# Kernel tuning notes

Measured on AMD Instinct MI355X. Metric: run time of the kernel, lower is better.

## Reference

```python
import jax, jax.numpy as jnp
import numpy as np

N_NODES = 50000
N_EDGES = 800000
NUM_GRAPHS = 250
NODES_PER_GRAPH = 200  # max_len for to_dense_batch
IN_DIM = 128
H1 = 128
H2 = 128
LSTM_H = 128
OUT_DIM = 2
NEG_SLOPE = 0.2  # PyG GATConv default leaky relu slope


def setup_inputs() -> dict:
    key = jax.random.key(0)
    ks = jax.random.split(key, 16)
    x = jax.random.normal(ks[0], (N_NODES, IN_DIM), dtype=jnp.float32)
    edge_index = jax.random.randint(ks[1], (2, N_EDGES), 0, N_NODES, dtype=jnp.int32)
    batch = (jnp.arange(N_NODES, dtype=jnp.int32) // NODES_PER_GRAPH)
    g = lambda k, shp, fan: jax.random.normal(k, shp, dtype=jnp.float32) / np.sqrt(fan)
    return {
        "x": x,
        "edge_index": edge_index,
        "batch": batch,
        "W_gat": g(ks[2], (IN_DIM, H1), IN_DIM),
        "a_src": g(ks[3], (H1,), H1),
        "a_dst": g(ks[4], (H1,), H1),
        "b_gat": jnp.zeros((H1,), jnp.float32),
        "W_gcn": g(ks[5], (H1, H2), H1),
        "b_gcn": jnp.zeros((H2,), jnp.float32),
        "W_ih": g(ks[6], (4 * LSTM_H, H2), H2),
        "W_hh": g(ks[7], (4 * LSTM_H, LSTM_H), LSTM_H),
        "b_ih": jnp.zeros((4 * LSTM_H,), jnp.float32),
        "b_hh": jnp.zeros((4 * LSTM_H,), jnp.float32),
        "W_fc": g(ks[8], (LSTM_H, OUT_DIM), LSTM_H),
        "b_fc": jnp.zeros((OUT_DIM,), jnp.float32),
    }


def _add_self_loops(edge_index, n):
    loop = jnp.arange(n, dtype=edge_index.dtype)
    src = jnp.concatenate([edge_index[0], loop])
    dst = jnp.concatenate([edge_index[1], loop])
    return src, dst


def _gat_conv(x, edge_index, W, a_src, a_dst, b):
    n = x.shape[0]
    h = x @ W                                  # [N, H1]
    src, dst = _add_self_loops(edge_index, n)
    alpha_s = h @ a_src                        # [N]
    alpha_d = h @ a_dst
    e = alpha_s[src] + alpha_d[dst]            # [E+N]
    e = jnp.where(e > 0, e, NEG_SLOPE * e)     # leaky relu
    # softmax over edges sharing the same destination node
    m = jax.ops.segment_max(e, dst, num_segments=n)
    ex = jnp.exp(e - m[dst])
    denom = jax.ops.segment_sum(ex, dst, num_segments=n)
    alpha = ex / denom[dst]
    out = jax.ops.segment_sum(h[src] * alpha[:, None], dst, num_segments=n)
    return out + b


def _gcn_conv(x, edge_index, W, b):
    n = x.shape[0]
    h = x @ W                                  # [N, H2]
    src, dst = _add_self_loops(edge_index, n)
    deg = jax.ops.segment_sum(jnp.ones_like(dst, dtype=h.dtype), dst, num_segments=n)
    dinv = jax.lax.rsqrt(jnp.maximum(deg, 1.0))
    coef = dinv[src] * dinv[dst]               # symmetric normalization
    out = jax.ops.segment_sum(h[src] * coef[:, None], dst, num_segments=n)
    return out + b


def _to_dense_batch(x, batch, num_graphs, max_len):
    n = x.shape[0]
    ones = jnp.ones((n,), jnp.int32)
    counts = jax.ops.segment_sum(ones, batch, num_segments=num_graphs)
    starts = jnp.cumsum(counts) - counts
    pos = jnp.arange(n, dtype=jnp.int32) - starts[batch]
    padded = jnp.zeros((num_graphs, max_len, x.shape[1]), x.dtype)
    padded = padded.at[batch, pos].set(x)
    return padded, counts


def _lstm_last_hidden(padded, lengths, W_ih, W_hh, b_ih, b_hh):
    B, T, D = padded.shape
    H = W_hh.shape[1]
    xs = jnp.swapaxes(padded, 0, 1)            # [T, B, D]

    def step(carry, x_t):
        h, c = carry
        gates = x_t @ W_ih.T + b_ih + h @ W_hh.T + b_hh
        i, f, g, o = jnp.split(gates, 4, axis=-1)
        c = jax.nn.sigmoid(f) * c + jax.nn.sigmoid(i) * jnp.tanh(g)
        h = jax.nn.sigmoid(o) * jnp.tanh(c)
        return (h, c), h

    init = (jnp.zeros((B, H), padded.dtype), jnp.zeros((B, H), padded.dtype))
    _, hs = jax.lax.scan(step, init, xs)       # hs: [T, B, H]
    # packed-sequence semantics: hidden state at each graph's last valid step
    return hs[lengths - 1, jnp.arange(B)]


def reference(x, edge_index, batch, W_gat, a_src, a_dst, b_gat, W_gcn, b_gcn,
              W_ih, W_hh, b_ih, b_hh, W_fc, b_fc):
    h = jax.nn.relu(_gat_conv(x, edge_index, W_gat, a_src, a_dst, b_gat))
    h = jax.nn.relu(_gcn_conv(h, edge_index, W_gcn, b_gcn))
    padded, lengths = _to_dense_batch(h, batch, NUM_GRAPHS, NODES_PER_GRAPH)
    g_rep = _lstm_last_hidden(padded, lengths, W_ih, W_hh, b_ih, b_hh)
    return g_rep @ W_fc + b_fc
```

## Files before the change

### kernel.cpp

```cpp
#include <hip/hip_runtime.h>
#include <cstddef>

#define NN 50000
#define NE 800000
#define NG 250
#define TT 200
#define DD 128
#define GH 512
#define NEG_SLOPE 0.2f
#define NCHUNK 4
#define CLEN 50
#define CAP 128
#define PSTRIDE 136

typedef __attribute__((ext_vector_type(8))) short bf16x8;
typedef __attribute__((ext_vector_type(4))) float f32x4;

static __device__ __forceinline__ float fsig(float x) { return 1.0f / (1.0f + __expf(-x)); }
static __device__ __forceinline__ float ftanh(float x) {
    float e = __expf(2.0f * x);
    return 1.0f - 2.0f / (e + 1.0f);
}
static __device__ __forceinline__ unsigned short f2bf(float f) {
    unsigned int u = __float_as_uint(f);
    return (unsigned short)((u + 0x7fffu + ((u >> 16) & 1u)) >> 16);
}
static __device__ __forceinline__ float bf2f(unsigned short b) {
    return __uint_as_float(((unsigned int)b) << 16);
}

static __device__ __forceinline__ void gll16(const float* src, float* ldsdst) {
    __builtin_amdgcn_global_load_lds(
        (const __attribute__((address_space(1))) void*)src,
        (__attribute__((address_space(3))) void*)ldsdst, 16, 0, 0);
}

__global__ void k_init(int* cnt, int* gstart, int n, int ng1) {
    int i = blockIdx.x * 256 + threadIdx.x;
    if (i < n) cnt[i] = 1;
    if (i < ng1) gstart[i] = n;
}

__global__ void k_transpose2(const float* __restrict__ inA, float* __restrict__ outA,
                             const float* __restrict__ inB, float* __restrict__ outB) {
    int b = blockIdx.x, k = threadIdx.x;
    if (b < DD) outA[b * DD + k] = inA[k * DD + b];
    else { int n = b - DD; outB[n * DD + k] = inB[k * DD + n]; }
}

__global__ __launch_bounds__(256) void k_gemm(
    const float* __restrict__ A, const float* __restrict__ B, float* __restrict__ C,
    int M, int N, int t0, int clen, int rowsPerGraph,
    const float* __restrict__ bias1, const float* __restrict__ bias2,
    unsigned short* __restrict__ Cbf,
    float* __restrict__ as_out, float* __restrict__ ad_out,
    const float* __restrict__ a_src, const float* __restrict__ a_dst)
{
    __shared__ float4 As[2][1024];
    __shared__ float4 Bs[2][1024];
    const int tid = threadIdx.x;
    const int wv = tid >> 6;
    const int m0 = blockIdx.x * 128, n0 = blockIdx.y * 128;
    const int tr = tid >> 4, tc = tid & 15;

    float acc[8][8];
    #pragma unroll
    for (int i = 0; i < 8; ++i)
        #pragma unroll
        for (int j = 0; j < 8; ++j) acc[i][j] = 0.f;

    auto stageA = [&](int buf, int k0) {
        #pragma unroll
        for (int it = 0; it < 4; ++it) {
            int f4 = it * 256 + tid;
            int r = f4 >> 3;
            int c4s = (f4 & 7) ^ (r & 7);
            int gr = m0 + r;
            float* dst = (float*)&As[buf][it * 256 + wv * 64];
            if (gr < M) {
                int flat = (gr / clen) * rowsPerGraph + t0 + (gr % clen);
                gll16(A + (size_t)flat * DD + k0 + c4s * 4, dst);
            }
        }
    };
    auto stageB = [&](int buf, int k0) {
        #pragma unroll
        for (int it = 0; it < 4; ++it) {
            int f4 = it * 256 + tid;
            int r = f4 >> 3;
            int c4s = (f4 & 7) ^ (r & 7);
            int gn = n0 + r;
            float* dst = (float*)&Bs[buf][it * 256 + wv * 64];
            if (gn < N) gll16(B + (size_t)gn * DD + k0 + c4s * 4, dst);
        }
    };

    stageA(0, 0); stageB(0, 0);
    __syncthreads();
    int buf = 0;
    const int axor = tr & 7;
    const int bxor = tc & 7;
    for (int ks = 0; ks < 4; ++ks) {
        if (ks < 3) { stageA(buf ^ 1, (ks + 1) * 32); stageB(buf ^ 1, (ks + 1) * 32); }
        const float4* Af = &As[buf][0];
        const float4* Bf = &Bs[buf][0];
        #pragma unroll 1
        for (int k4 = 0; k4 < 8; ++k4) {
            float4 a[8], b[8];
            #pragma unroll
            for (int i = 0; i < 8; ++i) a[i] = Af[(tr + i * 16) * 8 + (k4 ^ axor)];
            #pragma unroll
            for (int j = 0; j < 8; ++j) b[j] = Bf[(tc + j * 16) * 8 + (k4 ^ bxor)];
            #pragma unroll
            for (int i = 0; i < 8; ++i)
                #pragma unroll
                for (int j = 0; j < 8; ++j)
                    acc[i][j] += a[i].x * b[j].x + a[i].y * b[j].y + a[i].z * b[j].z + a[i].w * b[j].w;
        }
        __syncthreads();
        buf ^= 1;
    }

    if (as_out) {
        float asv[8], adv[8];
        #pragma unroll
        for (int j = 0; j < 8; ++j) { asv[j] = a_src[tc + 16 * j]; adv[j] = a_dst[tc + 16 * j]; }
        #pragma unroll
        for (int i = 0; i < 8; ++i) {
            float s = 0.f, d = 0.f;
            #pragma unroll
            for (int j = 0; j < 8; ++j) { s += acc[i][j] * asv[j]; d += acc[i][j] * adv[j]; }
            #pragma unroll
            for (int off = 1; off < 16; off <<= 1) { s += __shfl_xor(s, off); d += __shfl_xor(d, off); }
            int gr = m0 + tr + i * 16;
            if (tc == 0 && gr < M) { as_out[gr] = s; ad_out[gr] = d; }
        }
    }

    #pragma unroll
    for (int i = 0; i < 8; ++i) {
        int gr = m0 + tr + i * 16;
        if (gr >= M) continue;
        #pragma unroll
        for (int j = 0; j < 8; ++j) {
            int gn = n0 + tc + j * 16;
            if (gn >= N) continue;
            float v = acc[i][j];
            if (bias1) v += bias1[gn];
            if (bias2) v += bias2[gn];
            if (Cbf) Cbf[(size_t)gr * N + gn] = f2bf(v);
            else     C[(size_t)gr * N + gn] = v;
        }
    }
}

__global__ __launch_bounds__(256) void k_gemm_mx(
    const float* __restrict__ A, const float* __restrict__ Bw, float* __restrict__ C,
    int M, int N, const float* __restrict__ bias1, const float* __restrict__ bias2)
{
    __shared__ float4 As[4096];
    const int tid = threadIdx.x;
    const int wv = tid >> 6;
    const int l = tid & 63;
    const int m0 = blockIdx.x * 128, n0 = blockIdx.y * 128;
    const int wr = (wv >> 1) * 64, wc = (wv & 1) * 64;
    const int lr = l & 15, kg = l >> 4;

    #pragma unroll
    for (int it = 0; it < 16; ++it) {
        int f4 = it * 256 + tid;
        int r = f4 >> 5, c4 = f4 & 31;
        int c4s = c4 ^ (r & 7);
        int gr = m0 + r;
        float* dst = (float*)&As[it * 256 + wv * 64];
        if (gr < M) gll16(A + (size_t)gr * DD + c4s * 4, dst);
    }

    bf16x8 bh[4][4];
    #pragma unroll
    for (int ct = 0; ct < 4; ++ct) {
        const float* brow = Bw + (size_t)(n0 + wc + ct * 16 + lr) * DD;
        #pragma unroll
        for (int ks = 0; ks < 4; ++ks) {
            float4 f0 = *(const float4*)(brow + ks * 32 + kg * 8);
            float4 f1 = *(const float4*)(brow + ks * 32 + kg * 8 + 4);
            float ff[8] = {f0.x, f0.y, f0.z, f0.w, f1.x, f1.y, f1.z, f1.w};
            #pragma unroll
            for (int j = 0; j < 8; ++j) bh[ct][ks][j] = (short)f2bf(ff[j]);
        }
    }
    __syncthreads();

    f32x4 acc[4][4];
    #pragma unroll
    for (int rt = 0; rt < 4; ++rt)
        #pragma unroll
        for (int ct = 0; ct < 4; ++ct) acc[rt][ct] = (f32x4){0.f, 0.f, 0.f, 0.f};

    #pragma unroll 1
    for (int ks = 0; ks < 4; ++ks) {
        bf16x8 ahi[4], alo[4];
        #pragma unroll
        for (int rt = 0; rt < 4; ++rt) {
            int row = wr + rt * 16 + lr;
            int qb = ks * 8 + kg * 2;
            float4 f0 = As[row * 32 + (qb ^ (row & 7))];
            float4 f1 = As[row * 32 + ((qb + 1) ^ (row & 7))];
            float ff[8] = {f0.x, f0.y, f0.z, f0.w, f1.x, f1.y, f1.z, f1.w};
            #pragma unroll
            for (int j = 0; j < 8; ++j) {
                unsigned short hi = f2bf(ff[j]);
                ahi[rt][j] = (short)hi;
                alo[rt][j] = (short)f2bf(ff[j] - bf2f(hi));
            }
        }
        #pragma unroll
        for (int rt = 0; rt < 4; ++rt)
            #pragma unroll
            for (int ct = 0; ct < 4; ++ct) {
                acc[rt][ct] = __builtin_amdgcn_mfma_f32_16x16x32_bf16(ahi[rt], bh[ct][ks], acc[rt][ct], 0, 0, 0);
                acc[rt][ct] = __builtin_amdgcn_mfma_f32_16x16x32_bf16(alo[rt], bh[ct][ks], acc[rt][ct], 0, 0, 0);
            }
    }

    #pragma unroll
    for (int ct = 0; ct < 4; ++ct) {
        const float* brow = Bw + (size_t)(n0 + wc + ct * 16 + lr) * DD;
        #pragma unroll
        for (int ks = 0; ks < 4; ++ks) {
            float4 f0 = *(const float4*)(brow + ks * 32 + kg * 8);
            float4 f1 = *(const float4*)(brow + ks * 32 + kg * 8 + 4);
            float ff[8] = {f0.x, f0.y, f0.z, f0.w, f1.x, f1.y, f1.z, f1.w};
            #pragma unroll
            for (int j = 0; j < 8; ++j)
                bh[ct][ks][j] = (short)f2bf(ff[j] - bf2f(f2bf(ff[j])));
        }
    }

    #pragma unroll 1
    for (int ks = 0; ks < 4; ++ks) {
        bf16x8 ahi[4];
        #pragma unroll
        for (int rt = 0; rt < 4; ++rt) {
            int row = wr + rt * 16 + lr;
            int qb = ks * 8 + kg * 2;
            float4 f0 = As[row * 32 + (qb ^ (row & 7))];
            float4 f1 = As[row * 32 + ((qb + 1) ^ (row & 7))];
            float ff[8] = {f0.x, f0.y, f0.z, f0.w, f1.x, f1.y, f1.z, f1.w};
            #pragma unroll
            for (int j = 0; j < 8; ++j) ahi[rt][j] = (short)f2bf(ff[j]);
        }
        #pragma unroll
        for (int rt = 0; rt < 4; ++rt)
            #pragma unroll
            for (int ct = 0; ct < 4; ++ct)
                acc[rt][ct] = __builtin_amdgcn_mfma_f32_16x16x32_bf16(ahi[rt], bh[ct][ks], acc[rt][ct], 0, 0, 0);
    }

    #pragma unroll
    for (int ct = 0; ct < 4; ++ct) {
        int col = n0 + wc + ct * 16 + lr;
        float bsum = bias1[col] + bias2[col];
        #pragma unroll
        for (int rt = 0; rt < 4; ++rt) {
            #pragma unroll
            for (int r = 0; r < 4; ++r) {
                int row = m0 + wr + rt * 16 + kg * 4 + r;
                if (row < M) C[(size_t)row * N + col] = acc[rt][ct][r] + bsum;
            }
        }
    }
}

__global__ __launch_bounds__(256) void k_gemm_mx128(
    const float* __restrict__ A, const float* __restrict__ Bw,
    unsigned short* __restrict__ Cbf, int M,
    float* __restrict__ as_out, float* __restrict__ ad_out,
    const float* __restrict__ a_src, const float* __restrict__ a_dst)
{
    __shared__ float4 As[4096];
    const int tid = threadIdx.x;
    const int wv = tid >> 6;
    const int l = tid & 63;
    const int lr = l & 15, kg = l >> 4;
    const int m0 = blockIdx.x * 128;
    const int rowbase = wv * 32;

    #pragma unroll
    for (int it = 0; it < 16; ++it) {
        int f4 = it * 256 + tid;
        int r = f4 >> 5, c4 = f4 & 31;
        int c4s = c4 ^ (r & 7);
        int gr = m0 + r;
        float* dst = (float*)&As[it * 256 + wv * 64];
        if (gr < M) gll16(A + (size_t)gr * DD + c4s * 4, dst);
    }
    __syncthreads();

    f32x4 acc[2][8];
    #pragma unroll
    for (int rt = 0; rt < 2; ++rt)
        #pragma unroll
        for (int ct = 0; ct < 8; ++ct) acc[rt][ct] = (f32x4){0.f, 0.f, 0.f, 0.f};

    #pragma unroll 1
    for (int ks = 0; ks < 4; ++ks) {
        bf16x8 bh[8];
        #pragma unroll
        for (int ct = 0; ct < 8; ++ct) {
            const float* brow = Bw + (size_t)(ct * 16 + lr) * DD + ks * 32 + kg * 8;
            float4 f0 = *(const float4*)brow;
            float4 f1 = *(const float4*)(brow + 4);
            float ff[8] = {f0.x, f0.y, f0.z, f0.w, f1.x, f1.y, f1.z, f1.w};
            #pragma unroll
            for (int j = 0; j < 8; ++j) bh[ct][j] = (short)f2bf(ff[j]);
        }
        bf16x8 ahi[2], alo[2];
        #pragma unroll
        for (int rt = 0; rt < 2; ++rt) {
            int row = rowbase + rt * 16 + lr;
            int qb = ks * 8 + kg * 2;
            float4 f0 = As[row * 32 + (qb ^ (row & 7))];
            float4 f1 = As[row * 32 + ((qb + 1) ^ (row & 7))];
            float ff[8] = {f0.x, f0.y, f0.z, f0.w, f1.x, f1.y, f1.z, f1.w};
            #pragma unroll
            for (int j = 0; j < 8; ++j) {
                unsigned short hi = f2bf(ff[j]);
                ahi[rt][j] = (short)hi;
                alo[rt][j] = (short)f2bf(ff[j] - bf2f(hi));
            }
        }
        #pragma unroll
        for (int rt = 0; rt < 2; ++rt)
            #pragma unroll
            for (int ct = 0; ct < 8; ++ct) {
                acc[rt][ct] = __builtin_amdgcn_mfma_f32_16x16x32_bf16(ahi[rt], bh[ct], acc[rt][ct], 0, 0, 0);
                acc[rt][ct] = __builtin_amdgcn_mfma_f32_16x16x32_bf16(alo[rt], bh[ct], acc[rt][ct], 0, 0, 0);
            }
    }
    #pragma unroll 1
    for (int ks = 0; ks < 4; ++ks) {
        bf16x8 bl[8];
        #pragma unroll
        for (int ct = 0; ct < 8; ++ct) {
            const float* brow = Bw + (size_t)(ct * 16 + lr) * DD + ks * 32 + kg * 8;
            float4 f0 = *(const float4*)brow;
            float4 f1 = *(const float4*)(brow + 4);
            float ff[8] = {f0.x, f0.y, f0.z, f0.w, f1.x, f1.y, f1.z, f1.w};
            #pragma unroll
            for (int j = 0; j < 8; ++j)
                bl[ct][j] = (short)f2bf(ff[j] - bf2f(f2bf(ff[j])));
        }
        bf16x8 ahi[2];
        #pragma unroll
        for (int rt = 0; rt < 2; ++rt) {
            int row = rowbase + rt * 16 + lr;
            int qb = ks * 8 + kg * 2;
            float4 f0 = As[row * 32 + (qb ^ (row & 7))];
            float4 f1 = As[row * 32 + ((qb + 1) ^ (row & 7))];
            float ff[8] = {f0.x, f0.y, f0.z, f0.w, f1.x, f1.y, f1.z, f1.w};
            #pragma unroll
            for (int j = 0; j < 8; ++j) ahi[rt][j] = (short)f2bf(ff[j]);
        }
        #pragma unroll
        for (int rt = 0; rt < 2; ++rt)
            #pragma unroll
            for (int ct = 0; ct < 8; ++ct)
                acc[rt][ct] = __builtin_amdgcn_mfma_f32_16x16x32_bf16(ahi[rt], bl[ct], acc[rt][ct], 0, 0, 0);
    }

    #pragma unroll
    for (int rt = 0; rt < 2; ++rt)
        #pragma unroll
        for (int ct = 0; ct < 8; ++ct) {
            int row = m0 + rowbase + rt * 16 + kg * 4;
            int col = ct * 16 + lr;
            #pragma unroll
            for (int r = 0; r < 4; ++r)
                if (row + r < M) Cbf[(size_t)(row + r) * DD + col] = f2bf(acc[rt][ct][r]);
        }
    if (as_out) {
        #pragma unroll
        for (int rt = 0; rt < 2; ++rt)
            #pragma unroll
            for (int r = 0; r < 4; ++r) {
                float s = 0.f, d = 0.f;
                #pragma unroll
                for (int ct = 0; ct < 8; ++ct) {
                    int col = ct * 16 + lr;
                    s += acc[rt][ct][r] * a_src[col];
                    d += acc[rt][ct][r] * a_dst[col];
                }
                #pragma unroll
                for (int off = 1; off < 16; off <<= 1) {
                    s += __shfl_xor(s, off);
                    d += __shfl_xor(d, off);
                }
                int row = m0 + rowbase + rt * 16 + kg * 4 + r;
                if (lr == 0 && row < M) { as_out[row] = s; ad_out[row] = d; }
            }
    }
}

__global__ void k_hist(const int* __restrict__ ei, int* cnt, int E) {
    int e = blockIdx.x * 256 + threadIdx.x;
    if (e < E) atomicAdd(&cnt[ei[E + e]], 1);
}

__global__ __launch_bounds__(256) void k_scan1(const int* __restrict__ cnt, int* __restrict__ fill,
                                               int* __restrict__ bsum, int n) {
    __shared__ int wsum[4];
    int tid = threadIdx.x, lane = tid & 63, wv = tid >> 6;
    int i = blockIdx.x * 256 + tid;
    int v = (i < n) ? cnt[i] : 0;
    int sc = v;
    #pragma unroll
    for (int off = 1; off < 64; off <<= 1) {
        int t = __shfl_up(sc, off);
        if (lane >= off) sc += t;
    }
    if (lane == 63) wsum[wv] = sc;
    __syncthreads();
    int base = 0;
    if (wv > 0) base += wsum[0];
    if (wv > 1) base += wsum[1];
    if (wv > 2) base += wsum[2];
    if (i < n) fill[i] = base + sc - v;
    if (tid == 255) bsum[blockIdx.x] = base + sc;
}
__global__ __launch_bounds__(256) void k_scan2(int* __restrict__ bsum, int nb) {
    __shared__ int wsum[4];
    int tid = threadIdx.x, lane = tid & 63, wv = tid >> 6;
    int v = (tid < nb) ? bsum[tid] : 0;
    int sc = v;
    #pragma unroll
    for (int off = 1; off < 64; off <<= 1) {
        int t = __shfl_up(sc, off);
        if (lane >= off) sc += t;
    }
    if (lane == 63) wsum[wv] = sc;
    __syncthreads();
    int base = 0;
    if (wv > 0) base += wsum[0];
    if (wv > 1) base += wsum[1];
    if (wv > 2) base += wsum[2];
    if (tid < nb) bsum[tid] = base + sc - v;
}
__global__ void k_scan3(const int* __restrict__ bsum, const int* __restrict__ cnt,
                        int* __restrict__ rp, int* __restrict__ fill,
                        float* __restrict__ dinv, const int* __restrict__ batch,
                        int* __restrict__ gstart, int n) {
    int i = blockIdx.x * 256 + threadIdx.x;
    if (i >= n) return;
    int v = fill[i] + bsum[blockIdx.x];
    rp[i] = v;
    fill[i] = v;
    if (i == n - 1) rp[n] = v + cnt[i];
    dinv[i] = rsqrtf(fmaxf((float)cnt[i], 1.0f));
    int b = batch[i];
    if (i == 0 || batch[i - 1] != b) gstart[b] = i;
}

__global__ void k_fill(const int* __restrict__ ei, int* fill, int* esrc, int E, int N) {
    int i = blockIdx.x * 256 + threadIdx.x;
    if (i < E) {
        int s = ei[i], d = ei[E + i];
        int slot = atomicAdd(&fill[d], 1);
        esrc[slot] = s;
    } else if (i < E + N) {
        int v = i - E;
        int slot = atomicAdd(&fill[v], 1);
        esrc[slot] = v;
    }
}

__global__ __launch_bounds__(256) void k_gat(
    const unsigned int* __restrict__ h1b,
    const float* __restrict__ as, const float* __restrict__ ad_,
    const int* __restrict__ rp, const int* __restrict__ esrc,
    const float* __restrict__ bias, float* __restrict__ out, int n)
{
    __shared__ float2 ws_sh[4][CAP];
    int wv = threadIdx.x >> 6;
    int node = blockIdx.x * 4 + wv;
    int lane = threadIdx.x & 63;
    if (node >= n) return;
    int r0 = rp[node], r1 = rp[node + 1];
    int deg = r1 - r0;
    float adv = ad_[node];

    float sum = 0.f;
    for (int base = 0; base < deg; base += 64) {
        int idx = base + lane;
        float ex = 0.f;
        if (idx < deg) {
            int s = esrc[r0 + idx];
            float e = as[s] + adv;
            e = e > 0.f ? e : NEG_SLOPE * e;
            ex = __expf(e);
            if (idx < CAP) ws_sh[wv][idx] = make_float2(ex, __int_as_float(s));
        }
        sum += ex;
    }
    #pragma unroll
    for (int off = 1; off < 64; off <<= 1) sum += __shfl_xor(sum, off);
    float inv = 1.0f / sum;

    int nser = deg < CAP ? deg : CAP;
    int npad = (nser + 7) & ~7;
    for (int p = nser + lane; p < npad; p += 64)
        ws_sh[wv][p] = make_float2(0.f, __int_as_float(0));

    float ax = 0.f, ay = 0.f;
    float wa[8]; unsigned int va[8];
    #pragma unroll
    for (int u = 0; u < 8; ++u) {
        float2 t = ws_sh[wv][u];
        wa[u] = t.x; va[u] = h1b[(size_t)__float_as_int(t.y) * 64 + lane];
    }
    #pragma unroll 1
    for (int idx = 8; idx < npad; idx += 8) {
        float wb[8]; unsigned int vb[8];
        #pragma unroll
        for (int u = 0; u < 8; ++u) {
            float2 t = ws_sh[wv][idx + u];
            wb[u] = t.x; vb[u] = h1b[(size_t)__float_as_int(t.y) * 64 + lane];
        }
        #pragma unroll
        for (int u = 0; u < 8; ++u) {
            ax += wa[u] * __uint_as_float(va[u] << 16);
            ay += wa[u] * __uint_as_float(va[u] & 0xffff0000u);
        }
        #pragma unroll
        for (int u = 0; u < 8; ++u) { wa[u] = wb[u]; va[u] = vb[u]; }
    }
    #pragma unroll
    for (int u = 0; u < 8; ++u) {
        ax += wa[u] * __uint_as_float(va[u] << 16);
        ay += wa[u] * __uint_as_float(va[u] & 0xffff0000u);
    }

    for (int j = r0 + CAP; j < r1; ++j) {
        int s = esrc[j];
        float e = as[s] + adv;
        e = e > 0.f ? e : NEG_SLOPE * e;
        float w = __expf(e);
        unsigned int v = h1b[(size_t)s * 64 + lane];
        ax += w * __uint_as_float(v << 16);
        ay += w * __uint_as_float(v & 0xffff0000u);
    }
    float2 bv = *(const float2*)(bias + 2 * lane);
    float2 o;
    o.x = fmaxf(ax * inv + bv.x, 0.f);
    o.y = fmaxf(ay * inv + bv.y, 0.f);
    *(float2*)(out + (size_t)node * DD + 2 * lane) = o;
}

__global__ __launch_bounds__(256) void k_gcn(
    const unsigned int* __restrict__ h2b, const float* __restrict__ dinv,
    const int* __restrict__ rp, const int* __restrict__ esrc,
    const float* __restrict__ bias, const int* __restrict__ batch,
    const int* __restrict__ gstart, float* __restrict__ padded, int n)
{
    __shared__ float2 cs_sh[4][CAP];
    int wv = threadIdx.x >> 6;
    int node = blockIdx.x * 4 + wv;
    int lane = threadIdx.x & 63;
    if (node >= n) return;
    int r0 = rp[node], r1 = rp[node + 1];
    int deg = r1 - r0;
    float dn = dinv[node];

    for (int base = 0; base < deg; base += 64) {
        int idx = base + lane;
        if (idx < deg && idx < CAP) {
            int s = esrc[r0 + idx];
            cs_sh[wv][idx] = make_float2(dinv[s], __int_as_float(s));
        }
    }
    int nser = deg < CAP ? deg : CAP;
    int npad = (nser + 7) & ~7;
    for (int p = nser + lane; p < npad; p += 64)
        cs_sh[wv][p] = make_float2(0.f, __int_as_float(0));
    __syncthreads();

    float ax = 0.f, ay = 0.f;
    float wa[8]; unsigned int va[8];
    #pragma unroll
    for (int u = 0; u < 8; ++u) {
        float2 t = cs_sh[wv][u];
        wa[u] = t.x; va[u] = h2b[(size_t)__float_as_int(t.y) * 64 + lane];
    }
    #pragma unroll 1
    for (int idx = 8; idx < npad; idx += 8) {
        float wb[8]; unsigned int vb[8];
        #pragma unroll
        for (int u = 0; u < 8; ++u) {
            float2 t = cs_sh[wv][idx + u];
            wb[u] = t.x; vb[u] = h2b[(size_t)__float_as_int(t.y) * 64 + lane];
        }
        #pragma unroll
        for (int u = 0; u < 8; ++u) {
            ax += wa[u] * __uint_as_float(va[u] << 16);
            ay += wa[u] * __uint_as_float(va[u] & 0xffff0000u);
        }
        #pragma unroll
        for (int u = 0; u < 8; ++u) { wa[u] = wb[u]; va[u] = vb[u]; }
    }
    #pragma unroll
    for (int u = 0; u < 8; ++u) {
        ax += wa[u] * __uint_as_float(va[u] << 16);
        ay += wa[u] * __uint_as_float(va[u] & 0xffff0000u);
    }

    for (int j = r0 + CAP; j < r1; ++j) {
        int s = esrc[j];
        float c = dinv[s];
        unsigned int v = h2b[(size_t)s * 64 + lane];
        ax += c * __uint_as_float(v << 16);
        ay += c * __uint_as_float(v & 0xffff0000u);
    }
    int g = batch[node];
    if (g < 0 || g >= NG) return;
    int p = node - gstart[g];
    if (p < 0 || p >= TT) return;
    float2 bv = *(const float2*)(bias + 2 * lane);
    float2 o;
    o.x = fmaxf(ax * dn + bv.x, 0.f);
    o.y = fmaxf(ay * dn + bv.y, 0.f);
    *(float2*)(padded + ((size_t)g * TT + p) * DD + 2 * lane) = o;
}

__global__ __launch_bounds__(1024) void k_lstm8(
    const float* __restrict__ xw,
    const float* __restrict__ Whh,
    const int* __restrict__ gstart,
    float* __restrict__ grep)
{
    int g = blockIdx.x, tid = threadIdx.x;
    __shared__ __align__(16) float h_sh[DD];
    __shared__ __align__(16) float part[8][4 * PSTRIDE];

    const int seg = tid >> 7;
    const int gq  = tid & 127;
    const int qt  = gq >> 5;
    const int ub  = (gq & 31) * 4;
    const int u   = tid >> 2;
    const int q   = tid & 3;
    const int lane = tid & 63;
    const int qbase = lane & ~3;

    float4 w[4][4];
    #pragma unroll
    for (int g4 = 0; g4 < 4; ++g4)
        #pragma unroll
        for (int i = 0; i < 4; ++i)
            w[g4][i] = *(const float4*)(Whh + (size_t)(4 * gq + g4) * DD + seg * 16 + i * 4);

    float creg = 0.f, hn = 0.f;
    if (tid < DD) h_sh[tid] = 0.f;
    int take = gstart[g + 1] - gstart[g] - 1;
    if (take < 0) take = 0;
    if (take > TT - 1) take = TT - 1;
    __syncthreads();

    const float* xb = xw + (size_t)g * TT * GH + q * DD + (u & 127);
    float xv = (tid < 512) ? xb[0] : 0.f;

    for (int t = 0; t < TT; ++t) {
        float xvn = 0.f;
        if (tid < 512 && t + 1 < TT) xvn = xb[(size_t)(t + 1) * GH];

        float4 hseg[4];
        #pragma unroll
        for (int i = 0; i < 4; ++i) hseg[i] = *(const float4*)(h_sh + seg * 16 + i * 4);
        float p0 = 0.f, p1 = 0.f, p2 = 0.f, p3 = 0.f;
        #pragma unroll
        for (int i = 0; i < 4; ++i) {
            float4 h4 = hseg[i];
            p0 += h4.x * w[0][i].x + h4.y * w[0][i].y + h4.z * w[0][i].z + h4.w * w[0][i].w;
            p1 += h4.x * w[1][i].x + h4.y * w[1][i].y + h4.z * w[1][i].z + h4.w * w[1][i].w;
            p2 += h4.x * w[2][i].x + h4.y * w[2][i].y + h4.z * w[2][i].z + h4.w * w[2][i].w;
            p3 += h4.x * w[3][i].x + h4.y * w[3][i].y + h4.z * w[3][i].z + h4.w * w[3][i].w;
        }
        *(float4*)(&part[seg][qt * PSTRIDE + ub]) = make_float4(p0, p1, p2, p3);
        __syncthreads();

        if (tid < 512) {
            int pidx = q * PSTRIDE + u;
            float G = xv + ((part[0][pidx] + part[1][pidx]) + (part[2][pidx] + part[3][pidx]))
                         + ((part[4][pidx] + part[5][pidx]) + (part[6][pidx] + part[7][pidx]));
            float a = (q == 2) ? 2.f : -1.f;
            float e = __expf(a * G);
            float act = (q == 2) ? (1.f - 2.f / (e + 1.f)) : (1.f / (1.f + e));
            float ai = __shfl(act, qbase + 0);
            float af = __shfl(act, qbase + 1);
            float ag = __shfl(act, qbase + 2);
            float ao = __shfl(act, qbase + 3);
            creg = af * creg + ai * ag;
            hn = ao * ftanh(creg);
            if (q == 0) {
                h_sh[u] = hn;
                if (t == take) grep[g * DD + u] = hn;
            }
        }
        xv = xvn;
        __syncthreads();
    }
}

__global__ __launch_bounds__(512) void k_lstm(
    const float* __restrict__ xw, const float* __restrict__ Whh,
    const int* __restrict__ gstart,
    float* __restrict__ hstate, float* __restrict__ cstate,
    float* __restrict__ grep, int t0, int clen)
{
    int g = blockIdx.x, tid = threadIdx.x;
    __shared__ __align__(16) float h_sh[DD];
    __shared__ __align__(16) float part[4][4 * PSTRIDE];

    const int seg = tid >> 7;
    const int gq  = tid & 127;
    const int qt  = gq >> 5;
    const int ub  = (gq & 31) * 4;
    const int u   = tid >> 2;
    const int q   = tid & 3;
    const int lane = tid & 63;
    const int qbase = lane & ~3;

    float4 w[4][8];
    #pragma unroll
    for (int g4 = 0; g4 < 4; ++g4)
        #pragma unroll
        for (int i = 0; i < 8; ++i)
            w[g4][i] = *(const float4*)(Whh + (size_t)(4 * gq + g4) * DD + seg * 32 + i * 4);

    float creg = 0.f, hn = 0.f;
    if (t0 == 0) {
        if (tid < DD) h_sh[tid] = 0.f;
    } else {
        creg = cstate[g * DD + u];
        hn = hstate[g * DD + u];
        if (q == 0) h_sh[u] = hn;
    }
    int take = gstart[g + 1] - gstart[g] - 1;
    if (take < 0) take = 0;
    if (take > TT - 1) take = TT - 1;
    __syncthreads();

    const float* xb = xw + (size_t)g * clen * GH + q * DD + u;
    float xv = xb[0];

    for (int t = t0; t < t0 + clen; ++t) {
        int rel = t - t0;
        float xvn = 0.f;
        if (rel + 1 < clen) xvn = xb[(size_t)(rel + 1) * GH];

        float4 hseg[8];
        #pragma unroll
        for (int i = 0; i < 8; ++i) hseg[i] = *(const float4*)(h_sh + seg * 32 + i * 4);
        float p0 = 0.f, p1 = 0.f, p2 = 0.f, p3 = 0.f;
        #pragma unroll
        for (int i = 0; i < 8; ++i) {
            float4 h4 = hseg[i];
            p0 += h4.x * w[0][i].x + h4.y * w[0][i].y + h4.z * w[0][i].z + h4.w * w[0][i].w;
            p1 += h4.x * w[1][i].x + h4.y * w[1][i].y + h4.z * w[1][i].z + h4.w * w[1][i].w;
            p2 += h4.x * w[2][i].x + h4.y * w[2][i].y + h4.z * w[2][i].z + h4.w * w[2][i].w;
            p3 += h4.x * w[3][i].x + h4.y * w[3][i].y + h4.z * w[3][i].z + h4.w * w[3][i].w;
        }
        *(float4*)(&part[seg][qt * PSTRIDE + ub]) = make_float4(p0, p1, p2, p3);
        __syncthreads();

        int pidx = q * PSTRIDE + u;
        float G = xv + part[0][pidx] + part[1][pidx] + part[2][pidx] + part[3][pidx];
        float a = (q == 2) ? 2.f : -1.f;
        float e = __expf(a * G);
        float act = (q == 2) ? (1.f - 2.f / (e + 1.f)) : (1.f / (1.f + e));
        float ai = __shfl(act, qbase + 0);
        float af = __shfl(act, qbase + 1);
        float ag = __shfl(act, qbase + 2);
        float ao = __shfl(act, qbase + 3);
        creg = af * creg + ai * ag;
        hn = ao * ftanh(creg);
        if (q == 0) {
            h_sh[u] = hn;
            if (t == take) grep[g * DD + u] = hn;
        }
        xv = xvn;
        __syncthreads();
    }
    if (q == 0) { hstate[g * DD + u] = hn; cstate[g * DD + u] = creg; }
}

__global__ void k_fc(const float* __restrict__ grep, const float* __restrict__ Wfc,
                     const float* __restrict__ bfc, float* __restrict__ out, int G) {
    int i = blockIdx.x * 256 + threadIdx.x;
    if (i >= G * 2) return;
    int g = i >> 1, o = i & 1;
    float acc = bfc[o];
    for (int d = 0; d < DD; ++d) acc += grep[g * DD + d] * Wfc[d * 2 + o];
    out[i] = acc;
}

extern "C" void kernel_launch(void* const* d_in, const int* in_sizes, int n_in,
                              void* d_out, int out_size, void* d_ws, size_t ws_size,
                              hipStream_t stream) {
    const float* x     = (const float*)d_in[0];
    const int*   ei    = (const int*)d_in[1];
    const int*   batch = (const int*)d_in[2];
    const float* Wgat  = (const float*)d_in[3];
    const float* a_src = (const float*)d_in[4];
    const float* a_dst = (const float*)d_in[5];
    const float* b_gat = (const float*)d_in[6];
    const float* Wgcn  = (const float*)d_in[7];
    const float* b_gcn = (const float*)d_in[8];
    const float* Wih   = (const float*)d_in[9];
    const float* Whh   = (const float*)d_in[10];
    const float* b_ih  = (const float*)d_in[11];
    const float* b_hh  = (const float*)d_in[12];
    const float* Wfc   = (const float*)d_in[13];
    const float* b_fc  = (const float*)d_in[14];
    float* out = (float*)d_out;

    float* ws = (float*)d_ws;
    const size_t F = (size_t)NN * DD;
    unsigned short* h1b = (unsigned short*)ws;
    unsigned short* h2b = (unsigned short*)ws;
    float* xwChunk = ws;
    float* gato   = ws + F;
    float* padded = ws + F;
    size_t off = 2 * F;
    float* alpha_s = ws + off; off += 50048;
    float* alpha_d = ws + off; off += 50048;
    float* dinv    = ws + off; off += 50048;
    int*   cnt     = (int*)(ws + off); off += 50048;
    int*   rp      = (int*)(ws + off); off += 50056;
    int*   fill    = (int*)(ws + off); off += 50048;
    int*   esrc    = (int*)(ws + off); off += 850048;
    int*   bsum    = (int*)(ws + off); off += 256;
    int*   gstart  = (int*)(ws + off); off += 256;
    float* grep    = ws + off; off += 32000;
    float* hstate  = ws + off; off += 32000;
    float* cstate  = ws + off; off += 32000;
    float* WgatT   = ws + off; off += 16384;
    float* WgcnT   = ws + off; off += 16384;
    const size_t xwBigFloats = (size_t)NG * TT * GH;
    float* xwBig = ws + off;
    const bool big = ws_size >= (off + xwBigFloats) * sizeof(float);

    k_transpose2<<<256, 128, 0, stream>>>(Wgat, WgatT, Wgcn, WgcnT);

    if (big) {
        k_gemm_mx128<<<391, 256, 0, stream>>>(x, WgatT, h1b, NN,
                                              alpha_s, alpha_d, a_src, a_dst);
    } else {
        k_gemm<<<dim3(391, 1), 256, 0, stream>>>(x, WgatT, nullptr, NN, DD, 0, TT, TT,
                                                 nullptr, nullptr, h1b,
                                                 alpha_s, alpha_d, a_src, a_dst);
    }

    k_init<<<196, 256, 0, stream>>>(cnt, gstart, NN, NG + 1);
    k_hist<<<3125, 256, 0, stream>>>(ei, cnt, NE);
    k_scan1<<<196, 256, 0, stream>>>(cnt, fill, bsum, NN);
    k_scan2<<<1, 256, 0, stream>>>(bsum, 196);
    k_scan3<<<196, 256, 0, stream>>>(bsum, cnt, rp, fill, dinv, batch, gstart, NN);
    k_fill<<<3321, 256, 0, stream>>>(ei, fill, esrc, NE, NN);

    k_gat<<<12500, 256, 0, stream>>>((const unsigned int*)h1b, alpha_s, alpha_d,
                                     rp, esrc, b_gat, gato, NN);

    if (big) {
        k_gemm_mx128<<<391, 256, 0, stream>>>(gato, WgcnT, h2b, NN,
                                              nullptr, nullptr, nullptr, nullptr);
    } else {
        k_gemm<<<dim3(391, 1), 256, 0, stream>>>(gato, WgcnT, nullptr, NN, DD, 0, TT, TT,
                                                 nullptr, nullptr, h2b,
                                                 nullptr, nullptr, nullptr, nullptr);
    }

    k_gcn<<<12500, 256, 0, stream>>>((const unsigned int*)h2b, dinv, rp, esrc,
                                     b_gcn, batch, gstart, padded, NN);

    if (big) {
        k_gemm_mx<<<dim3(391, 4), 256, 0, stream>>>(padded, Wih, xwBig, NG * TT, GH,
                                                    b_ih, b_hh);
        k_lstm8<<<NG, 1024, 0, stream>>>(xwBig, Whh, gstart, grep);
    } else {
        for (int c = 0; c < NCHUNK; ++c) {
            int t0 = c * CLEN;
            k_gemm<<<dim3(98, 4), 256, 0, stream>>>(padded, Wih, xwChunk, NG * CLEN, GH,
                                                    t0, CLEN, TT, b_ih, b_hh,
                                                    nullptr, nullptr, nullptr, nullptr, nullptr);
            k_lstm<<<NG, 512, 0, stream>>>(xwChunk, Whh, gstart, hstate, cstate, grep, t0, CLEN);
        }
    }

    k_fc<<<2, 256, 0, stream>>>(grep, Wfc, b_fc, out, NG);
}
```

Before: 559.6 us.

## Loop GEMM over all output column groups per block and stage stores via LDS

The input-projection GEMM now launches one block per 128-row tile and loops over all four 128-column groups, so the A tile is loaded into LDS once instead of four times across separate blocks. Results are staged through a padded LDS buffer so global stores are coalesced float4 row writes. The 1024-thread LSTM kernel is removed and the big path uses the 512-thread LSTM kernel over the full sequence. This cuts grid parallelism to 391 blocks and raises LDS use per block, which may lower occupancy.

```diff
diff --git a/kernel.cpp b/kernel.cpp
--- a/kernel.cpp
+++ b/kernel.cpp
@@ -12,6 +12,7 @@
 #define CLEN 50
 #define CAP 128
 #define PSTRIDE 136
+#define CSTRIDE 132
 
 typedef __attribute__((ext_vector_type(8))) short bf16x8;
 typedef __attribute__((ext_vector_type(4))) float f32x4;
@@ -156,13 +157,14 @@
 
 __global__ __launch_bounds__(256) void k_gemm_mx(
     const float* __restrict__ A, const float* __restrict__ Bw, float* __restrict__ C,
-    int M, int N, const float* __restrict__ bias1, const float* __restrict__ bias2)
+    int M, const float* __restrict__ bias1, const float* __restrict__ bias2)
 {
     __shared__ float4 As[4096];
+    __shared__ float  Cs[128 * CSTRIDE];
     const int tid = threadIdx.x;
     const int wv = tid >> 6;
     const int l = tid & 63;
-    const int m0 = blockIdx.x * 128, n0 = blockIdx.y * 128;
+    const int m0 = blockIdx.x * 128;
     const int wr = (wv >> 1) * 64, wc = (wv & 1) * 64;
     const int lr = l & 15, kg = l >> 4;
 
@@ -175,99 +177,109 @@
         float* dst = (float*)&As[it * 256 + wv * 64];
         if (gr < M) gll16(A + (size_t)gr * DD + c4s * 4, dst);
     }
-
-    bf16x8 bh[4][4];
-    #pragma unroll
-    for (int ct = 0; ct < 4; ++ct) {
-        const float* brow = Bw + (size_t)(n0 + wc + ct * 16 + lr) * DD;
-        #pragma unroll
+    __syncthreads();
+
+    #pragma unroll 1
+    for (int cg = 0; cg < 4; ++cg) {
+        const int n0 = cg * 128;
+        f32x4 acc[4][4];
+        #pragma unroll
+        for (int rt = 0; rt < 4; ++rt)
+            #pragma unroll
+            for (int ct = 0; ct < 4; ++ct) acc[rt][ct] = (f32x4){0.f, 0.f, 0.f, 0.f};
+
+        bf16x8 bh[4][4];
+        #pragma unroll
+        for (int ct = 0; ct < 4; ++ct) {
+            const float* brow = Bw + (size_t)(n0 + wc + ct * 16 + lr) * DD;
+            #pragma unroll
+            for (int ks = 0; ks < 4; ++ks) {
+                float4 f0 = *(const float4*)(brow + ks * 32 + kg * 8);
+                float4 f1 = *(const float4*)(brow + ks * 32 + kg * 8 + 4);
+                float ff[8] = {f0.x, f0.y, f0.z, f0.w, f1.x, f1.y, f1.z, f1.w};
+                #pragma unroll
+                for (int j = 0; j < 8; ++j) bh[ct][ks][j] = (short)f2bf(ff[j]);
+            }
+        }
+        #pragma unroll 1
         for (int ks = 0; ks < 4; ++ks) {
-            float4 f0 = *(const float4*)(brow + ks * 32 + kg * 8);
-            float4 f1 = *(const float4*)(brow + ks * 32 + kg * 8 + 4);
-            float ff[8] = {f0.x, f0.y, f0.z, f0.w, f1.x, f1.y, f1.z, f1.w};
-            #pragma unroll
-            for (int j = 0; j < 8; ++j) bh[ct][ks][j] = (short)f2bf(ff[j]);
-        }
-    }
-    __syncthreads();
-
-    f32x4 acc[4][4];
-    #pragma unroll
-    for (int rt = 0; rt < 4; ++rt)
-        #pragma unroll
-        for (int ct = 0; ct < 4; ++ct) acc[rt][ct] = (f32x4){0.f, 0.f, 0.f, 0.f};
-
-    #pragma unroll 1
-    for (int ks = 0; ks < 4; ++ks) {
-        bf16x8 ahi[4], alo[4];
-        #pragma unroll
-        for (int rt = 0; rt < 4; ++rt) {
-            int row = wr + rt * 16 + lr;
-            int qb = ks * 8 + kg * 2;
-            float4 f0 = As[row * 32 + (qb ^ (row & 7))];
-            float4 f1 = As[row * 32 + ((qb + 1) ^ (row & 7))];
-            float ff[8] = {f0.x, f0.y, f0.z, f0.w, f1.x, f1.y, f1.z, f1.w};
-            #pragma unroll
-            for (int j = 0; j < 8; ++j) {
-                unsigned short hi = f2bf(ff[j]);
-                ahi[rt][j] = (short)hi;
-                alo[rt][j] = (short)f2bf(ff[j] - bf2f(hi));
+            bf16x8 ahi[4], alo[4];
+            #pragma unroll
+            for (int rt = 0; rt < 4; ++rt) {
+                int row = wr + rt * 16 + lr;
+                int qb = ks * 8 + kg * 2;
+                float4 f0 = As[row * 32 + (qb ^ (row & 7))];
+                float4 f1 = As[row * 32 + ((qb + 1) ^ (row & 7))];
+                float ff[8] = {f0.x, f0.y, f0.z, f0.w, f1.x, f1.y, f1.z, f1.w};
+                #pragma unroll
+                for (int j = 0; j < 8; ++j) {
+                    unsigned short hi = f2bf(ff[j]);
+                    ahi[rt][j] = (short)hi;
+                    alo[rt][j] = (short)f2bf(ff[j] - bf2f(hi));
+                }
             }
-        }
-        #pragma unroll
-        for (int rt = 0; rt < 4; ++rt)
-            #pragma unroll
-            for (int ct = 0; ct < 4; ++ct) {
-                acc[rt][ct] = __builtin_amdgcn_mfma_f32_16x16x32_bf16(ahi[rt], bh[ct][ks], acc[rt][ct], 0, 0, 0);
-                acc[rt][ct] = __builtin_amdgcn_mfma_f32_16x16x32_bf16(alo[rt], bh[ct][ks], acc[rt][ct], 0, 0, 0);
+            #pragma unroll
+            for (int rt = 0; rt < 4; ++rt)
+                #pragma unroll
+                for (int ct = 0; ct < 4; ++ct) {
+                    acc[rt][ct] = __builtin_amdgcn_mfma_f32_16x16x32_bf16(ahi[rt], bh[ct][ks], acc[rt][ct], 0, 0, 0);
+                    acc[rt][ct] = __builtin_amdgcn_mfma_f32_16x16x32_bf16(alo[rt], bh[ct][ks], acc[rt][ct], 0, 0, 0);
+                }
+        }
+        #pragma unroll
+        for (int ct = 0; ct < 4; ++ct) {
+            const float* brow = Bw + (size_t)(n0 + wc + ct * 16 + lr) * DD;
+            #pragma unroll
+            for (int ks = 0; ks < 4; ++ks) {
+                float4 f0 = *(const float4*)(brow + ks * 32 + kg * 8);
+                float4 f1 = *(const float4*)(brow + ks * 32 + kg * 8 + 4);
+                float ff[8] = {f0.x, f0.y, f0.z, f0.w, f1.x, f1.y, f1.z, f1.w};
+                #pragma unroll
+                for (int j = 0; j < 8; ++j)
+                    bh[ct][ks][j] = (short)f2bf(ff[j] - bf2f(f2bf(ff[j])));
             }
-    }
-
-    #pragma unroll
-    for (int ct = 0; ct < 4; ++ct) {
-        const float* brow = Bw + (size_t)(n0 + wc + ct * 16 + lr) * DD;
-        #pragma unroll
+        }
+        #pragma unroll 1
         for (int ks = 0; ks < 4; ++ks) {
-            float4 f0 = *(const float4*)(brow + ks * 32 + kg * 8);
-            float4 f1 = *(const float4*)(brow + ks * 32 + kg * 8 + 4);
-            float ff[8] = {f0.x, f0.y, f0.z, f0.w, f1.x, f1.y, f1.z, f1.w};
-            #pragma unroll
-            for (int j = 0; j < 8; ++j)
-                bh[ct][ks][j] = (short)f2bf(ff[j] - bf2f(f2bf(ff[j])));
-        }
-    }
-
-    #pragma unroll 1
-    for (int ks = 0; ks < 4; ++ks) {
-        bf16x8 ahi[4];
-        #pragma unroll
-        for (int rt = 0; rt < 4; ++rt) {
-            int row = wr + rt * 16 + lr;
-            int qb = ks * 8 + kg * 2;
-            float4 f0 = As[row * 32 + (qb ^ (row & 7))];
-            float4 f1 = As[row * 32 + ((qb + 1) ^ (row & 7))];
-            float ff[8] = {f0.x, f0.y, f0.z, f0.w, f1.x, f1.y, f1.z, f1.w};
-            #pragma unroll
-            for (int j = 0; j < 8; ++j) ahi[rt][j] = (short)f2bf(ff[j]);
-        }
-        #pragma unroll
-        for (int rt = 0; rt < 4; ++rt)
-            #pragma unroll
-            for (int ct = 0; ct < 4; ++ct)
-                acc[rt][ct] = __builtin_amdgcn_mfma_f32_16x16x32_bf16(ahi[rt], bh[ct][ks], acc[rt][ct], 0, 0, 0);
-    }
-
-    #pragma unroll
-    for (int ct = 0; ct < 4; ++ct) {
-        int col = n0 + wc + ct * 16 + lr;
-        float bsum = bias1[col] + bias2[col];
-        #pragma unroll
-        for (int rt = 0; rt < 4; ++rt) {
-            #pragma unroll
-            for (int r = 0; r < 4; ++r) {
-                int row = m0 + wr + rt * 16 + kg * 4 + r;
-                if (row < M) C[(size_t)row * N + col] = acc[rt][ct][r] + bsum;
+            bf16x8 ahi[4];
+            #pragma unroll
+            for (int rt = 0; rt < 4; ++rt) {
+                int row = wr + rt * 16 + lr;
+                int qb = ks * 8 + kg * 2;
+                float4 f0 = As[row * 32 + (qb ^ (row & 7))];
+                float4 f1 = As[row * 32 + ((qb + 1) ^ (row & 7))];
+                float ff[8] = {f0.x, f0.y, f0.z, f0.w, f1.x, f1.y, f1.z, f1.w};
+                #pragma unroll
+                for (int j = 0; j < 8; ++j) ahi[rt][j] = (short)f2bf(ff[j]);
             }
+            #pragma unroll
+            for (int rt = 0; rt < 4; ++rt)
+                #pragma unroll
+                for (int ct = 0; ct < 4; ++ct)
+                    acc[rt][ct] = __builtin_amdgcn_mfma_f32_16x16x32_bf16(ahi[rt], bh[ct][ks], acc[rt][ct], 0, 0, 0);
+        }
+
+        __syncthreads();
+        #pragma unroll
+        for (int ct = 0; ct < 4; ++ct) {
+            int col = wc + ct * 16 + lr;
+            float bsum = bias1[n0 + col] + bias2[n0 + col];
+            #pragma unroll
+            for (int rt = 0; rt < 4; ++rt) {
+                int row = wr + rt * 16 + kg * 4;
+                #pragma unroll
+                for (int r = 0; r < 4; ++r)
+                    Cs[(row + r) * CSTRIDE + col] = acc[rt][ct][r] + bsum;
+            }
+        }
+        __syncthreads();
+        #pragma unroll
+        for (int it = 0; it < 16; ++it) {
+            int f4 = it * 256 + tid;
+            int r = f4 >> 5, c4 = f4 & 31;
+            int gr = m0 + r;
+            if (gr < M)
+                *(float4*)(C + (size_t)gr * GH + n0 + c4 * 4) = *(const float4*)(&Cs[r * CSTRIDE + c4 * 4]);
         }
     }
 }
@@ -629,84 +641,6 @@
     o.x = fmaxf(ax * dn + bv.x, 0.f);
     o.y = fmaxf(ay * dn + bv.y, 0.f);
     *(float2*)(padded + ((size_t)g * TT + p) * DD + 2 * lane) = o;
-}
-
-__global__ __launch_bounds__(1024) void k_lstm8(
-    const float* __restrict__ xw,
-    const float* __restrict__ Whh,
-    const int* __restrict__ gstart,
-    float* __restrict__ grep)
-{
-    int g = blockIdx.x, tid = threadIdx.x;
-    __shared__ __align__(16) float h_sh[DD];
-    __shared__ __align__(16) float part[8][4 * PSTRIDE];
-
-    const int seg = tid >> 7;
-    const int gq  = tid & 127;
-    const int qt  = gq >> 5;
-    const int ub  = (gq & 31) * 4;
-    const int u   = tid >> 2;
-    const int q   = tid & 3;
-    const int lane = tid & 63;
-    const int qbase = lane & ~3;
-
-    float4 w[4][4];
-    #pragma unroll
-    for (int g4 = 0; g4 < 4; ++g4)
-        #pragma unroll
-        for (int i = 0; i < 4; ++i)
-            w[g4][i] = *(const float4*)(Whh + (size_t)(4 * gq + g4) * DD + seg * 16 + i * 4);
-
-    float creg = 0.f, hn = 0.f;
-    if (tid < DD) h_sh[tid] = 0.f;
-    int take = gstart[g + 1] - gstart[g] - 1;
-    if (take < 0) take = 0;
-    if (take > TT - 1) take = TT - 1;
-    __syncthreads();
-
-    const float* xb = xw + (size_t)g * TT * GH + q * DD + (u & 127);
-    float xv = (tid < 512) ? xb[0] : 0.f;
-
-    for (int t = 0; t < TT; ++t) {
-        float xvn = 0.f;
-        if (tid < 512 && t + 1 < TT) xvn = xb[(size_t)(t + 1) * GH];
-
-        float4 hseg[4];
-        #pragma unroll
-        for (int i = 0; i < 4; ++i) hseg[i] = *(const float4*)(h_sh + seg * 16 + i * 4);
-        float p0 = 0.f, p1 = 0.f, p2 = 0.f, p3 = 0.f;
-        #pragma unroll
-        for (int i = 0; i < 4; ++i) {
-            float4 h4 = hseg[i];
-            p0 += h4.x * w[0][i].x + h4.y * w[0][i].y + h4.z * w[0][i].z + h4.w * w[0][i].w;
-            p1 += h4.x * w[1][i].x + h4.y * w[1][i].y + h4.z * w[1][i].z + h4.w * w[1][i].w;
-            p2 += h4.x * w[2][i].x + h4.y * w[2][i].y + h4.z * w[2][i].z + h4.w * w[2][i].w;
-            p3 += h4.x * w[3][i].x + h4.y * w[3][i].y + h4.z * w[3][i].z + h4.w * w[3][i].w;
-        }
-        *(float4*)(&part[seg][qt * PSTRIDE + ub]) = make_float4(p0, p1, p2, p3);
-        __syncthreads();
-
-        if (tid < 512) {
-            int pidx = q * PSTRIDE + u;
-            float G = xv + ((part[0][pidx] + part[1][pidx]) + (part[2][pidx] + part[3][pidx]))
-                         + ((part[4][pidx] + part[5][pidx]) + (part[6][pidx] + part[7][pidx]));
-            float a = (q == 2) ? 2.f : -1.f;
-            float e = __expf(a * G);
-            float act = (q == 2) ? (1.f - 2.f / (e + 1.f)) : (1.f / (1.f + e));
-            float ai = __shfl(act, qbase + 0);
-            float af = __shfl(act, qbase + 1);
-            float ag = __shfl(act, qbase + 2);
-            float ao = __shfl(act, qbase + 3);
-            creg = af * creg + ai * ag;
-            hn = ao * ftanh(creg);
-            if (q == 0) {
-                h_sh[u] = hn;
-                if (t == take) grep[g * DD + u] = hn;
-            }
-        }
-        xv = xvn;
-        __syncthreads();
-    }
 }
 
 __global__ __launch_bounds__(512) void k_lstm(
@@ -882,9 +816,8 @@
                                      b_gcn, batch, gstart, padded, NN);
 
     if (big) {
-        k_gemm_mx<<<dim3(391, 4), 256, 0, stream>>>(padded, Wih, xwBig, NG * TT, GH,
-                                                    b_ih, b_hh);
-        k_lstm8<<<NG, 1024, 0, stream>>>(xwBig, Whh, gstart, grep);
+        k_gemm_mx<<<391, 256, 0, stream>>>(padded, Wih, xwBig, NG * TT, b_ih, b_hh);
+        k_lstm<<<NG, 512, 0, stream>>>(xwBig, Whh, gstart, hstate, cstate, grep, 0, TT);
     } else {
         for (int c = 0; c < NCHUNK; ++c) {
             int t0 = c * CLEN;
```

New measurement: 556.1 us. About the same (-0.6%).
